# Performance work log

Hardware: AMD Instinct MI355X
Metric: run time of the kernel (lower is better)

Reference implementation:

```python
import jax, jax.numpy as jnp
import numpy as np

N_PREV = 8191
DIMS = 4096


def setup_inputs() -> dict:
    key = jax.random.key(0)
    k1, k2, k3, k4, k5 = jax.random.split(key, 5)
    prev_inps = jax.random.normal(k1, (N_PREV, DIMS), dtype=jnp.float32)
    inp = jax.random.normal(k2, (DIMS,), dtype=jnp.float32)
    # learned parameters, init std=0.01 as in the torch module
    W_Q = jax.random.normal(k3, (DIMS, DIMS), dtype=jnp.float32) * 0.01
    W_K = jax.random.normal(k4, (DIMS, DIMS), dtype=jnp.float32) * 0.01
    W_V = jax.random.normal(k5, (DIMS, DIMS), dtype=jnp.float32) * 0.01
    return {"prev_inps": prev_inps, "inp": inp, "W_Q": W_Q, "W_K": W_K, "W_V": W_V}


def reference(prev_inps, inp, W_Q, W_K, W_V):
    # One masked self-attention decode step.
    inputs = jnp.concatenate([prev_inps, inp[None, :]], axis=0)  # (n+1, d)
    query = W_Q @ inp                                            # (d,)
    keys = jnp.einsum('md,nd->nm', W_K, inputs)                  # (n+1, d)
    values = jnp.einsum('md,nd->nm', W_V, inputs)                # (n+1, d)
    logits = keys @ query                                        # (n+1,)
    aweights = jax.nn.softmax(logits, axis=-1)                   # (n+1,)
    context = aweights @ values                                  # (d,)
    output = context + inp                                       # residual
    return (output, inputs)
```

## Files before the change

### kernel.cpp

```cpp
#include <hip/hip_runtime.h>
#include <math.h>

#define D      4096
#define NPREV  8191
#define NROWS  8192
#define FBL    2048
#define FRL    4
#define PFB    128

typedef float f4 __attribute__((ext_vector_type(4)));

static __device__ __forceinline__ void nt_store4(f4 v, float* p) {
    __builtin_nontemporal_store(v, reinterpret_cast<f4*>(p));
}
static __device__ __forceinline__ f4 ld4(const float* p) {
    return *reinterpret_cast<const f4*>(p);
}
static __device__ __forceinline__ void st4(f4 v, float* p) {
    *reinterpret_cast<f4*>(p) = v;
}

__global__ void k_qkq(const float* __restrict__ W_Q, const float* __restrict__ W_K,
                      const float* __restrict__ inp, float* __restrict__ kqpart) {
    __shared__ f4 s_inp[1024];
    __shared__ float s_q[16];
    int t = threadIdx.x, b = blockIdx.x;
    int wid = t >> 6, lane = t & 63;
    for (int i = t; i < 1024; i += 256) s_inp[i] = ld4(inp + 4 * i);
    __syncthreads();
    #pragma unroll
    for (int j = 0; j < 4; ++j) {
        int r = 4 * wid + j;
        const float* Wrow = W_Q + (size_t)(16 * b + r) * D;
        float acc = 0.f;
        #pragma unroll
        for (int i = 0; i < 16; ++i) {
            int c = lane + 64 * i;
            f4 w = ld4(Wrow + 4 * c);
            f4 x = s_inp[c];
            acc += w.x * x.x + w.y * x.y + w.z * x.z + w.w * x.w;
        }
        #pragma unroll
        for (int off = 32; off; off >>= 1) acc += __shfl_down(acc, off, 64);
        if (lane == 0) s_q[r] = acc;
    }
    __syncthreads();
    f4 a0 = (f4)0.f, a1 = a0, a2 = a0, a3 = a0;
    #pragma unroll
    for (int r = 0; r < 16; ++r) {
        const float* Wrow = W_K + (size_t)(16 * b + r) * D;
        float qm = s_q[r];
        a0 += qm * ld4(Wrow + 4 * t);
        a1 += qm * ld4(Wrow + 4 * (t + 256));
        a2 += qm * ld4(Wrow + 4 * (t + 512));
        a3 += qm * ld4(Wrow + 4 * (t + 768));
    }
    float* kp = kqpart + (size_t)b * D;
    st4(a0, kp + 4 * t);          st4(a1, kp + 4 * (t + 256));
    st4(a2, kp + 4 * (t + 512));  st4(a3, kp + 4 * (t + 768));
}

__global__ void k_kqred(const float* __restrict__ kqpart, float* __restrict__ kq) {
    int d = blockIdx.x * 256 + threadIdx.x;
    float a0 = 0.f, a1 = 0.f, a2 = 0.f, a3 = 0.f;
    for (int p = 0; p < 256; p += 4) {
        a0 += kqpart[(size_t)p * D + d];
        a1 += kqpart[(size_t)(p + 1) * D + d];
        a2 += kqpart[(size_t)(p + 2) * D + d];
        a3 += kqpart[(size_t)(p + 3) * D + d];
    }
    kq[d] = (a0 + a1) + (a2 + a3);
}

__global__ __launch_bounds__(1024, 8) void k_flash_lds(
        const float* __restrict__ prev, const float* __restrict__ inp,
        const float* __restrict__ kq, float* __restrict__ io,
        float* __restrict__ ms, float* __restrict__ ctxpart,
        const float* __restrict__ W_V, float* __restrict__ sink) {
    if ((int)blockIdx.x >= FBL) {
        int pb = (int)blockIdx.x - FBL;
        f4 s = (f4)0.f;
        for (size_t i = (size_t)pb * 1024 + threadIdx.x;
             i < (size_t)D * (D / 4); i += (size_t)PFB * 1024)
            s += ld4(W_V + 4 * i);
        float v = s.x + s.y + s.z + s.w;
        if (v > 1e30f) sink[threadIdx.x] = v;
        return;
    }
    __shared__ f4 s_x[FRL][1024];
    __shared__ float s_wred[16][FRL];
    __shared__ float s_log[FRL];
    const int n0 = blockIdx.x * FRL;
    const int t = threadIdx.x;
    const int wid = t >> 6, lane = t & 63;
    const f4 kqv = ld4(kq + 4 * t);

    f4 x[FRL];
    #pragma unroll
    for (int r = 0; r < FRL; ++r) {
        int n = n0 + r;
        const float* src = (n < NPREV) ? (prev + (size_t)n * D) : inp;
        x[r] = ld4(src + 4 * t);
    }
    float p[FRL];
    #pragma unroll
    for (int r = 0; r < FRL; ++r) {
        int n = n0 + r;
        nt_store4(x[r], io + (size_t)n * D + 4 * t);
        s_x[r][t] = x[r];
        p[r] = x[r].x * kqv.x + x[r].y * kqv.y + x[r].z * kqv.z + x[r].w * kqv.w;
    }
    #pragma unroll
    for (int r = 0; r < FRL; ++r) {
        float v = p[r];
        #pragma unroll
        for (int off = 32; off; off >>= 1) v += __shfl_down(v, off, 64);
        if (lane == 0) s_wred[wid][r] = v;
    }
    __syncthreads();
    if (t < FRL) {
        float s = 0.f;
        #pragma unroll
        for (int w = 0; w < 16; ++w) s += s_wred[w][t];
        s_log[t] = s;
    }
    __syncthreads();
    float m_b = -INFINITY;
    #pragma unroll
    for (int r = 0; r < FRL; ++r) m_b = fmaxf(m_b, s_log[r]);
    float e[FRL], s_b = 0.f;
    #pragma unroll
    for (int r = 0; r < FRL; ++r) { e[r] = __expf(s_log[r] - m_b); s_b += e[r]; }
    f4 a = (f4)0.f;
    #pragma unroll
    for (int r = 0; r < FRL; ++r) a += e[r] * s_x[r][t];
    st4(a, ctxpart + (size_t)blockIdx.x * D + 4 * t);
    if (t == 0) { ms[2 * blockIdx.x] = m_b; ms[2 * blockIdx.x + 1] = s_b; }
}

template<int FBT>
__global__ void k_combine(const float* __restrict__ ms, const float* __restrict__ ctxpart,
                          float* __restrict__ ctx) {
    constexpr int PPT = FBT / 256;
    constexpr int PPG = FBT / 16;
    __shared__ float s_w[FBT];
    __shared__ float s_red[8];
    __shared__ f4 s_acc[16][16];
    int t = threadIdx.x;
    int lane = t & 63, wid = t >> 6;
    float mloc[PPT];
    float mx = -INFINITY;
    #pragma unroll
    for (int k = 0; k < PPT; ++k) { mloc[k] = ms[2 * (t + 256 * k)]; mx = fmaxf(mx, mloc[k]); }
    #pragma unroll
    for (int off = 32; off; off >>= 1) mx = fmaxf(mx, __shfl_down(mx, off, 64));
    if (lane == 0) s_red[wid] = mx;
    __syncthreads();
    float M = fmaxf(fmaxf(s_red[0], s_red[1]), fmaxf(s_red[2], s_red[3]));
    float sc = 0.f;
    #pragma unroll
    for (int k = 0; k < PPT; ++k) {
        float w = __expf(mloc[k] - M);
        s_w[t + 256 * k] = w;
        sc += w * ms[2 * (t + 256 * k) + 1];
    }
    #pragma unroll
    for (int off = 32; off; off >>= 1) sc += __shfl_down(sc, off, 64);
    if (lane == 0) s_red[4 + wid] = sc;
    __syncthreads();
    float S = s_red[4] + s_red[5] + s_red[6] + s_red[7];
    int c = t & 15, g = t >> 4;
    int col4 = blockIdx.x * 16 + c;
    f4 a = (f4)0.f;
    #pragma unroll 8
    for (int i = 0; i < PPG; ++i) {
        int pp = g * PPG + i;
        a += s_w[pp] * ld4(ctxpart + (size_t)pp * D + 4 * col4);
    }
    s_acc[g][c] = a;
    __syncthreads();
    if (t < 16) {
        f4 aa = (f4)0.f;
        #pragma unroll
        for (int gg = 0; gg < 16; ++gg) aa += s_acc[gg][t];
        st4(aa * (1.f / S), ctx + 4 * (blockIdx.x * 16 + t));
    }
}

__global__ void k_matvec_out(const float* __restrict__ W, const float* __restrict__ v,
                             const float* __restrict__ resid, float* __restrict__ out) {
    int row  = blockIdx.x * 4 + (threadIdx.x >> 6);
    int lane = threadIdx.x & 63;
    const float* Wrow = W + (size_t)row * D;
    float acc = 0.f;
    #pragma unroll
    for (int i = 0; i < 16; ++i) {
        int c = lane + i * 64;
        f4 w = ld4(Wrow + 4 * c);
        f4 x = ld4(v + 4 * c);
        acc += w.x * x.x + w.y * x.y + w.z * x.z + w.w * x.w;
    }
    #pragma unroll
    for (int off = 32; off; off >>= 1) acc += __shfl_down(acc, off, 64);
    if (lane == 0) out[row] = acc + resid[row];
}

extern "C" void kernel_launch(void* const* d_in, const int* in_sizes, int n_in,
                              void* d_out, int out_size, void* d_ws, size_t ws_size,
                              hipStream_t stream) {
    const float* prev = (const float*)d_in[0];
    const float* inp  = (const float*)d_in[1];
    const float* W_Q  = (const float*)d_in[2];
    const float* W_K  = (const float*)d_in[3];
    const float* W_V  = (const float*)d_in[4];
    float* out = (float*)d_out;
    float* io  = out + D;
    float* ws  = (float*)d_ws;

    float* kqpart  = ws;
    float* kq      = kqpart + (size_t)256 * D;
    float* ms      = kq + D;
    float* ctxpart = ms + 2 * FBL;
    float* ctx     = ctxpart + (size_t)FBL * D;
    float* sink    = ctx + D;

    k_qkq<<<256, 256, 0, stream>>>(W_Q, W_K, inp, kqpart);
    k_kqred<<<16, 256, 0, stream>>>(kqpart, kq);
    k_flash_lds<<<FBL + PFB, 1024, 0, stream>>>(prev, inp, kq, io, ms, ctxpart,
                                                W_V, sink);
    k_combine<FBL><<<64, 256, 0, stream>>>(ms, ctxpart, ctx);
    k_matvec_out<<<1024, 256, 0, stream>>>(W_V, ctx, inp, out);
}
```

Baseline: 132.7 us.

## Drop W_V L2 prefetch blocks and use nontemporal loads for weight streams

Removes the extra prefetch blocks in the flash kernel that streamed W_V through the cache so the final matvec could hit in cache. Weight loads in the QK and output matvecs now use nontemporal loads to avoid polluting the cache. It also adds a fallback path with a smaller workspace that computes q and kq via separate kernels. Losing the W_V prefetch means the final matvec must read W_V from HBM again, which may cost more than the bandwidth saved in the flash kernel.

```diff
diff --git a/kernel.cpp b/kernel.cpp
--- a/kernel.cpp
+++ b/kernel.cpp
@@ -6,10 +6,12 @@
 #define NROWS  8192
 #define FBL    2048
 #define FRL    4
-#define PFB    128
 
 typedef float f4 __attribute__((ext_vector_type(4)));
 
+static __device__ __forceinline__ f4 nt_load4(const float* p) {
+    return __builtin_nontemporal_load(reinterpret_cast<const f4*>(p));
+}
 static __device__ __forceinline__ void nt_store4(f4 v, float* p) {
     __builtin_nontemporal_store(v, reinterpret_cast<f4*>(p));
 }
@@ -36,7 +38,7 @@
         #pragma unroll
         for (int i = 0; i < 16; ++i) {
             int c = lane + 64 * i;
-            f4 w = ld4(Wrow + 4 * c);
+            f4 w = nt_load4(Wrow + 4 * c);
             f4 x = s_inp[c];
             acc += w.x * x.x + w.y * x.y + w.z * x.z + w.w * x.w;
         }
@@ -50,10 +52,10 @@
     for (int r = 0; r < 16; ++r) {
         const float* Wrow = W_K + (size_t)(16 * b + r) * D;
         float qm = s_q[r];
-        a0 += qm * ld4(Wrow + 4 * t);
-        a1 += qm * ld4(Wrow + 4 * (t + 256));
-        a2 += qm * ld4(Wrow + 4 * (t + 512));
-        a3 += qm * ld4(Wrow + 4 * (t + 768));
+        a0 += qm * nt_load4(Wrow + 4 * t);
+        a1 += qm * nt_load4(Wrow + 4 * (t + 256));
+        a2 += qm * nt_load4(Wrow + 4 * (t + 512));
+        a3 += qm * nt_load4(Wrow + 4 * (t + 768));
     }
     float* kp = kqpart + (size_t)b * D;
     st4(a0, kp + 4 * t);          st4(a1, kp + 4 * (t + 256));
@@ -72,21 +74,55 @@
     kq[d] = (a0 + a1) + (a2 + a3);
 }
 
+template<bool RESIDUAL>
+__global__ void k_matvec_rows(const float* __restrict__ W, const float* __restrict__ v,
+                              const float* __restrict__ resid, float* __restrict__ out) {
+    int row  = blockIdx.x * 4 + (threadIdx.x >> 6);
+    int lane = threadIdx.x & 63;
+    const float* Wrow = W + (size_t)row * D;
+    float acc = 0.f;
+    #pragma unroll
+    for (int i = 0; i < 16; ++i) {
+        int c = lane + i * 64;
+        f4 w = nt_load4(Wrow + 4 * c);
+        f4 x = ld4(v + 4 * c);
+        acc += w.x * x.x + w.y * x.y + w.z * x.z + w.w * x.w;
+    }
+    #pragma unroll
+    for (int off = 32; off; off >>= 1) acc += __shfl_down(acc, off, 64);
+    if (lane == 0) out[row] = RESIDUAL ? (acc + resid[row]) : acc;
+}
+
+__global__ void k_kq(const float* __restrict__ W, const float* __restrict__ q,
+                     float* __restrict__ kq) {
+    __shared__ float s_q[D];
+    __shared__ f4 s_part[64][4];
+    int t = threadIdx.x;
+    int b = blockIdx.x;
+    for (int i = t; i < D; i += 256) s_q[i] = q[i];
+    __syncthreads();
+    int c4 = b * 4 + (t & 3);
+    int r0 = t >> 2;
+    f4 acc = (f4)0.f;
+    #pragma unroll 16
+    for (int i = 0; i < 64; ++i) {
+        int m = r0 + i * 64;
+        acc += s_q[m] * nt_load4(W + (size_t)m * D + 4 * c4);
+    }
+    s_part[r0][t & 3] = acc;
+    __syncthreads();
+    if (t < 4) {
+        f4 a = (f4)0.f;
+        #pragma unroll
+        for (int g = 0; g < 64; ++g) a += s_part[g][t];
+        st4(a, kq + 4 * (b * 4 + t));
+    }
+}
+
 __global__ __launch_bounds__(1024, 8) void k_flash_lds(
         const float* __restrict__ prev, const float* __restrict__ inp,
         const float* __restrict__ kq, float* __restrict__ io,
-        float* __restrict__ ms, float* __restrict__ ctxpart,
-        const float* __restrict__ W_V, float* __restrict__ sink) {
-    if ((int)blockIdx.x >= FBL) {
-        int pb = (int)blockIdx.x - FBL;
-        f4 s = (f4)0.f;
-        for (size_t i = (size_t)pb * 1024 + threadIdx.x;
-             i < (size_t)D * (D / 4); i += (size_t)PFB * 1024)
-            s += ld4(W_V + 4 * i);
-        float v = s.x + s.y + s.z + s.w;
-        if (v > 1e30f) sink[threadIdx.x] = v;
-        return;
-    }
+        float* __restrict__ ms, float* __restrict__ ctxpart) {
     __shared__ f4 s_x[FRL][1024];
     __shared__ float s_wred[16][FRL];
     __shared__ float s_log[FRL];
@@ -187,24 +223,6 @@
     }
 }
 
-__global__ void k_matvec_out(const float* __restrict__ W, const float* __restrict__ v,
-                             const float* __restrict__ resid, float* __restrict__ out) {
-    int row  = blockIdx.x * 4 + (threadIdx.x >> 6);
-    int lane = threadIdx.x & 63;
-    const float* Wrow = W + (size_t)row * D;
-    float acc = 0.f;
-    #pragma unroll
-    for (int i = 0; i < 16; ++i) {
-        int c = lane + i * 64;
-        f4 w = ld4(Wrow + 4 * c);
-        f4 x = ld4(v + 4 * c);
-        acc += w.x * x.x + w.y * x.y + w.z * x.z + w.w * x.w;
-    }
-    #pragma unroll
-    for (int off = 32; off; off >>= 1) acc += __shfl_down(acc, off, 64);
-    if (lane == 0) out[row] = acc + resid[row];
-}
-
 extern "C" void kernel_launch(void* const* d_in, const int* in_sizes, int n_in,
                               void* d_out, int out_size, void* d_ws, size_t ws_size,
                               hipStream_t stream) {
@@ -217,17 +235,32 @@
     float* io  = out + D;
     float* ws  = (float*)d_ws;
 
-    float* kqpart  = ws;
-    float* kq      = kqpart + (size_t)256 * D;
-    float* ms      = kq + D;
-    float* ctxpart = ms + 2 * FBL;
-    float* ctx     = ctxpart + (size_t)FBL * D;
-    float* sink    = ctx + D;
-
-    k_qkq<<<256, 256, 0, stream>>>(W_Q, W_K, inp, kqpart);
-    k_kqred<<<16, 256, 0, stream>>>(kqpart, kq);
-    k_flash_lds<<<FBL + PFB, 1024, 0, stream>>>(prev, inp, kq, io, ms, ctxpart,
-                                                W_V, sink);
-    k_combine<FBL><<<64, 256, 0, stream>>>(ms, ctxpart, ctx);
-    k_matvec_out<<<1024, 256, 0, stream>>>(W_V, ctx, inp, out);
-}
+    size_t need_fused = (size_t)((size_t)256 * D + D + 2 * FBL
+                                 + (size_t)FBL * D + D) * sizeof(float);
+
+    if (ws_size >= need_fused) {
+        float* kqpart  = ws;
+        float* kq      = kqpart + (size_t)256 * D;
+        float* ms      = kq + D;
+        float* ctxpart = ms + 2 * FBL;
+        float* ctx     = ctxpart + (size_t)FBL * D;
+
+        k_qkq<<<256, 256, 0, stream>>>(W_Q, W_K, inp, kqpart);
+        k_kqred<<<16, 256, 0, stream>>>(kqpart, kq);
+        k_flash_lds<<<FBL, 1024, 0, stream>>>(prev, inp, kq, io, ms, ctxpart);
+        k_combine<FBL><<<64, 256, 0, stream>>>(ms, ctxpart, ctx);
+        k_matvec_rows<true><<<1024, 256, 0, stream>>>(W_V, ctx, inp, out);
+    } else {
+        float* q       = ws;
+        float* kq      = q + D;
+        float* ms      = kq + D;
+        float* ctxpart = ms + 2 * FBL;
+        float* ctx     = ctxpart + (size_t)FBL * D;
+
+        k_matvec_rows<false><<<1024, 256, 0, stream>>>(W_Q, inp, nullptr, q);
+        k_kq<<<256, 256, 0, stream>>>(W_K, q, kq);
+        k_flash_lds<<<FBL, 1024, 0, stream>>>(prev, inp, kq, io, ms, ctxpart);
+        k_combine<FBL><<<64, 256, 0, stream>>>(ms, ctxpart, ctx);
+        k_matvec_rows<true><<<1024, 256, 0, stream>>>(W_V, ctx, inp, out);
+    }
+}
```

New measurement: 116.1 us. -12.5%, faster.
